# Kernel optimization log

Hardware: AMD Instinct MI355X
Metric: run time of the kernel (lower is better)

## Reference

```python
import jax, jax.numpy as jnp
import numpy as np

B, T, D, H, L, FF, SPLIT = 2, 4096, 256, 4 * 0 + 8, 4, 1024, 2048
HD = D // H
EPS = 1e-5


def _layernorm(x, s, b):
    mu = jnp.mean(x, axis=-1, keepdims=True)
    var = jnp.mean(jnp.square(x - mu), axis=-1, keepdims=True)
    return (x - mu) * jax.lax.rsqrt(var + EPS) * s + b


def setup_inputs() -> dict:
    key = jax.random.key(0)
    ks = jax.random.split(key, 10)
    sc = 0.02
    inp = {
        "rows": jax.random.normal(ks[0], (B, T, D), jnp.float32),
        "train_target_embeddings": jax.random.normal(ks[1], (B, SPLIT, D), jnp.float32),
        "Wq": sc * jax.random.normal(ks[2], (L, D, D), jnp.float32),
        "bq": jnp.zeros((L, D), jnp.float32),
        "Wk": sc * jax.random.normal(ks[3], (L, D, D), jnp.float32),
        "bk": jnp.zeros((L, D), jnp.float32),
        "Wv": sc * jax.random.normal(ks[4], (L, D, D), jnp.float32),
        "bv": jnp.zeros((L, D), jnp.float32),
        "Wo": sc * jax.random.normal(ks[5], (L, D, D), jnp.float32),
        "bo": jnp.zeros((L, D), jnp.float32),
        "W1": sc * jax.random.normal(ks[6], (L, D, FF), jnp.float32),
        "b1": jnp.zeros((L, FF), jnp.float32),
        "W2": sc * jax.random.normal(ks[7], (L, FF, D), jnp.float32),
        "b2": jnp.zeros((L, D), jnp.float32),
        "ln1_s": jnp.ones((L, D), jnp.float32),
        "ln1_b": jnp.zeros((L, D), jnp.float32),
        "ln2_s": jnp.ones((L, D), jnp.float32),
        "ln2_b": jnp.zeros((L, D), jnp.float32),
        "split": SPLIT,
    }
    return inp


def reference(rows, train_target_embeddings, Wq, bq, Wk, bk, Wv, bv, Wo, bo,
              W1, b1, W2, b2, ln1_s, ln1_b, ln2_s, ln2_b, split):
    # residual add of train target embeddings onto the train rows
    x = rows.at[:, :split, :].add(train_target_embeddings)
    t = x.shape[1]
    # allowed mask: every query can see all train columns; test queries also see themselves
    key_is_train = jnp.arange(t) < split                      # [T]
    allowed = key_is_train[None, :] | jnp.eye(t, dtype=bool)  # [T,T]
    neg = jnp.asarray(-1e9, x.dtype)
    scale = 1.0 / np.sqrt(HD)
    n_layers = Wq.shape[0]
    for l in range(n_layers):
        # multi-head attention with structured mask
        q = (x @ Wq[l] + bq[l]).reshape(x.shape[0], t, H, HD)
        k = (x @ Wk[l] + bk[l]).reshape(x.shape[0], t, H, HD)
        v = (x @ Wv[l] + bv[l]).reshape(x.shape[0], t, H, HD)
        logits = jnp.einsum('bqhd,bkhd->bhqk', q, k) * scale
        logits = jnp.where(allowed[None, None], logits, neg)
        attn = jax.nn.softmax(logits, axis=-1)
        o = jnp.einsum('bhqk,bkhd->bqhd', attn, v).reshape(x.shape[0], t, D)
        x = _layernorm(x + (o @ Wo[l] + bo[l]), ln1_s[l], ln1_b[l])
        # feed-forward
        h = jax.nn.gelu(x @ W1[l] + b1[l])
        x = _layernorm(x + (h @ W2[l] + b2[l]), ln2_s[l], ln2_b[l])
    return x
```

## Files before the change

### kernel.cpp

```cpp
#include <hip/hip_runtime.h>
#include <cstdint>
#include <cstddef>

#define TSEQ 4096
#define BATCH 2
#define DIM 256
#define NHEAD 8
#define HDIM 32
#define NLAYER 4
#define FFDIM 1024
#define SPLITN 2048
#define MROWS (BATCH * TSEQ)

#define QSCALE 0.2550784545f

typedef __attribute__((ext_vector_type(4))) float f32x4;
typedef __attribute__((ext_vector_type(8))) short bf16x8;

__device__ __forceinline__ short f2bf(float f) {
  union { float f; uint32_t u; } v; v.f = f;
  uint32_t r = v.u + 0x7fffu + ((v.u >> 16) & 1u);
  return (short)(r >> 16);
}

__device__ __forceinline__ float bf2f(short s) {
  union { uint32_t u; float f; } v; v.u = ((uint32_t)(uint16_t)s) << 16;
  return v.f;
}

__device__ __forceinline__ float fast_exp2(float x) {
#if __has_builtin(__builtin_amdgcn_exp2f)
  return __builtin_amdgcn_exp2f(x);
#else
  float r;
  asm volatile("v_exp_f32 %0, %1\n\ts_nop 1" : "=v"(r) : "v"(x));
  return r;
#endif
}

__device__ __forceinline__ uint32_t pack2bf(float a, float b) {
  union { float f; uint32_t u; } ua, ub; ua.f = a; ub.f = b;
  return ((ua.u + 0x8000u) >> 16) | ((ub.u + 0x8000u) & 0xffff0000u);
}

__device__ __forceinline__ bf16x8 mk8(uint32_t a, uint32_t b, uint32_t c, uint32_t d) {
  union { uint32_t u[4]; bf16x8 v; } x; x.u[0] = a; x.u[1] = b; x.u[2] = c; x.u[3] = d;
  return x.v;
}

__device__ __forceinline__ float gelu_f(float x) {
  float u = 0.7978845608f * x * (1.0f + 0.044715f * x * x);
  u = fminf(fmaxf(u, -20.f), 20.f);
  float e = fast_exp2(2.885390082f * u);
  float t = (e - 1.0f) / (e + 1.0f);
  return 0.5f * x * (1.0f + t);
}

#define AS1 __attribute__((address_space(1)))
#define AS3 __attribute__((address_space(3)))
__device__ __forceinline__ void gload16(const void* g, void* l) {
  __builtin_amdgcn_global_load_lds((AS1 void*)g, (AS3 void*)l, 16, 0, 0);
}

__global__ __launch_bounds__(256) void prep_w(
    const float* __restrict__ Wq, const float* __restrict__ Wk,
    const float* __restrict__ Wv, const float* __restrict__ Wo,
    const float* __restrict__ W1, const float* __restrict__ W2,
    short* __restrict__ qkvT, short* __restrict__ woT,
    short* __restrict__ w1T, short* __restrict__ w2T)
{
  const int NQKV = NLAYER * 768 * DIM;
  const int NO   = NLAYER * DIM * DIM;
  const int NF   = NLAYER * FFDIM * DIM;
  const int total = NQKV + NO + 2 * NF;
  for (int idx = blockIdx.x * 256 + threadIdx.x; idx < total; idx += gridDim.x * 256) {
    if (idx < NQKV) {
      const int l = idx / (768 * DIM);
      const int rem = idx - l * 768 * DIM;
      const int n = rem >> 8, k = rem & 255;
      const float* src = (n < 256) ? Wq : ((n < 512) ? Wk : Wv);
      qkvT[idx] = f2bf(src[((size_t)l * DIM + k) * DIM + (n & 255)]);
    } else if (idx < NQKV + NO) {
      const int j = idx - NQKV;
      const int l = j >> 16;
      const int rem = j & 65535;
      const int n = rem >> 8, k = rem & 255;
      woT[j] = f2bf(Wo[((size_t)l * DIM + k) * DIM + n]);
    } else if (idx < NQKV + NO + NF) {
      const int j = idx - NQKV - NO;
      const int l = j >> 18;
      const int rem = j & 262143;
      const int n = rem >> 8, k = rem & 255;
      w1T[j] = f2bf(W1[((size_t)l * DIM + k) * FFDIM + n]);
    } else {
      const int j = idx - NQKV - NO - NF;
      const int l = j >> 18;
      const int rem = j & 262143;
      const int n = rem >> 10, k = rem & 1023;
      w2T[j] = f2bf(W2[((size_t)l * FFDIM + k) * DIM + n]);
    }
  }
}

__global__ __launch_bounds__(256) void prep_x(
    const float* __restrict__ rows, const float* __restrict__ tte,
    float* __restrict__ xf, short* __restrict__ xb)
{
  const size_t idx = (size_t)blockIdx.x * 256 + threadIdx.x;
  float4 v = ((const float4*)rows)[idx];
  const size_t e = idx * 4;
  const int m = (int)(e >> 8);
  const int d = (int)(e & 255);
  const int t = m & (TSEQ - 1);
  const int bb = m >> 12;
  if (t < SPLITN) {
    const float4 a = ((const float4*)tte)[((size_t)bb * SPLITN + t) * (DIM / 4) + (d >> 2)];
    v.x += a.x; v.y += a.y; v.z += a.z; v.w += a.w;
  }
  ((float4*)xf)[idx] = v;
  short4 pk; pk.x = f2bf(v.x); pk.y = f2bf(v.y); pk.z = f2bf(v.z); pk.w = f2bf(v.w);
  ((short4*)xb)[idx] = pk;
}

#define GBM 128
#define GBN 64
#define GBK 64

template<int EPI>
__global__ __launch_bounds__(256, 4) void gemm_bt(
    const short* __restrict__ A, const short* __restrict__ BT,
    const float* __restrict__ bias0, const float* __restrict__ bias1,
    const float* __restrict__ bias2, void* __restrict__ Cout,
    int M, int N, int K)
{
  __shared__ short As[GBM * GBK];
  __shared__ short Bs[GBN * GBK];
  const int tid = threadIdx.x;
  const int lane = tid & 63;
  const int wave = tid >> 6;
  const int wm = wave & 1, wn = wave >> 1;
  const int col = lane & 15, quad = lane >> 4;

  const short* Ab = A + (size_t)blockIdx.x * GBM * K;
  const short* Bb = BT + (size_t)blockIdx.y * GBN * K;

  const f32x4 fz = {0.f, 0.f, 0.f, 0.f};
  f32x4 acc[4][2];
#pragma unroll
  for (int i = 0; i < 4; ++i)
#pragma unroll
    for (int j = 0; j < 2; ++j) acc[i][j] = fz;

  for (int k0 = 0; k0 < K; k0 += GBK) {
#pragma unroll
    for (int p = 0; p < 4; ++p) {
      const int i = p * 256 + tid;
      const int r = i >> 3, g = i & 7;
      gload16(Ab + (size_t)r * K + k0 + ((g ^ (r & 7)) * 8), &As[i * 8]);
    }
#pragma unroll
    for (int p = 0; p < 2; ++p) {
      const int i = p * 256 + tid;
      const int r = i >> 3, g = i & 7;
      gload16(Bb + (size_t)r * K + k0 + ((g ^ (r & 7)) * 8), &Bs[i * 8]);
    }
    __syncthreads();
#pragma unroll
    for (int ks = 0; ks < GBK; ks += 32) {
      bf16x8 af[4], bfr[2];
      const int gq = (ks >> 3) + quad;
#pragma unroll
      for (int tm = 0; tm < 4; ++tm) {
        const int row = wm * 64 + tm * 16 + col;
        af[tm] = *(const bf16x8*)&As[row * GBK + ((gq ^ (row & 7)) * 8)];
      }
#pragma unroll
      for (int tn = 0; tn < 2; ++tn) {
        const int row = wn * 32 + tn * 16 + col;
        bfr[tn] = *(const bf16x8*)&Bs[row * GBK + ((gq ^ (row & 7)) * 8)];
      }
#pragma unroll
      for (int tm = 0; tm < 4; ++tm)
#pragma unroll
        for (int tn = 0; tn < 2; ++tn)
          acc[tm][tn] = __builtin_amdgcn_mfma_f32_16x16x32_bf16(af[tm], bfr[tn], acc[tm][tn], 0, 0, 0);
    }
    __syncthreads();
  }

#pragma unroll
  for (int tm = 0; tm < 4; ++tm) {
    const int mbase = blockIdx.x * GBM + wm * 64 + tm * 16 + quad * 4;
#pragma unroll
    for (int tn = 0; tn < 2; ++tn) {
      const int n = blockIdx.y * GBN + wn * 32 + tn * 16 + col;
      float bv;
      if (EPI == 1) bv = (n < 256) ? bias0[n] : ((n < 512) ? bias1[n - 256] : bias2[n - 512]);
      else          bv = bias0[n];
#pragma unroll
      for (int r = 0; r < 4; ++r) {
        float v = acc[tm][tn][r] + bv;
        size_t off = (size_t)(mbase + r) * N + n;
        if (EPI == 1) {
          if (n < 256) v *= QSCALE;
          ((short*)Cout)[off] = f2bf(v);
        } else {
          ((short*)Cout)[off] = f2bf(gelu_f(v));
        }
      }
    }
  }
}

__global__ __launch_bounds__(256, 2) void gemm_ln(
    const short* __restrict__ A,
    const short* __restrict__ BT, const float* __restrict__ bias,
    const float* __restrict__ xres,
    const float* __restrict__ gs, const float* __restrict__ gb,
    float* __restrict__ xoutf, short* __restrict__ xoutb, int K)
{
  __shared__ short As[2][16 * 64];
  __shared__ short Bs[2][256 * 64];
  __shared__ float ssum[4][16], ssq[4][16];
  const int tid = threadIdx.x;
  const int lane = tid & 63;
  const int wave = tid >> 6;
  const int col = lane & 15, quad = lane >> 4;
  const int m0 = blockIdx.x * 16;

  const f32x4 fz = {0.f, 0.f, 0.f, 0.f};
  f32x4 acc[4];
#pragma unroll
  for (int j = 0; j < 4; ++j) acc[j] = fz;

  const int arow = (tid >> 3) & 15;
  const int agr  = tid & 7;
  const int grow = m0 + arow;
  const int asw  = (agr ^ (arow & 7)) * 8;

#define STAGE_B(k0_, buf_) do {                                              \
    _Pragma("unroll")                                                        \
    for (int p_ = 0; p_ < 8; ++p_) {                                         \
      const int i_ = p_ * 256 + tid;                                         \
      const int r_ = i_ >> 3, g_ = i_ & 7;                                   \
      gload16(BT + (size_t)r_ * K + (k0_) + ((g_ ^ (r_ & 7)) * 8),           \
              &Bs[buf_][i_ * 8]);                                            \
    } } while (0)

#define STAGE_A(k0_, buf_) do {                                              \
    if (tid < 128)                                                           \
      gload16(A + (size_t)grow * K + (k0_) + asw, &As[buf_][tid * 8]);       \
    } while (0)

  const int NT = K / 64;
  STAGE_B(0, 0);
  STAGE_A(0, 0);
  __syncthreads();

  int cur = 0;
  for (int t = 0; t < NT; ++t) {
    if (t + 1 < NT) {
      STAGE_B((t + 1) * 64, cur ^ 1);
      STAGE_A((t + 1) * 64, cur ^ 1);
    }
#pragma unroll
    for (int ks = 0; ks < 64; ks += 32) {
      bf16x8 af, bfr[4];
      const int gq = (ks >> 3) + quad;
      af = *(const bf16x8*)&As[cur][col * 64 + ((gq ^ (col & 7)) * 8)];
#pragma unroll
      for (int tn = 0; tn < 4; ++tn) {
        const int row = wave * 64 + tn * 16 + col;
        bfr[tn] = *(const bf16x8*)&Bs[cur][row * 64 + ((gq ^ (row & 7)) * 8)];
      }
#pragma unroll
      for (int tn = 0; tn < 4; ++tn)
        acc[tn] = __builtin_amdgcn_mfma_f32_16x16x32_bf16(af, bfr[tn], acc[tn], 0, 0, 0);
    }
    __syncthreads();
    cur ^= 1;
  }
#undef STAGE_B
#undef STAGE_A

  const float* resb = xres + (size_t)m0 * DIM;
#pragma unroll
  for (int tn = 0; tn < 4; ++tn) {
    const int n = wave * 64 + tn * 16 + col;
    const float bv = bias[n];
#pragma unroll
    for (int r = 0; r < 4; ++r) {
      const int row = quad * 4 + r;
      acc[tn][r] += bv + resb[(size_t)row * DIM + n];
    }
  }

#pragma unroll
  for (int r = 0; r < 4; ++r) {
    float s = 0.f, q = 0.f;
#pragma unroll
    for (int tn = 0; tn < 4; ++tn) { const float v = acc[tn][r]; s += v; q += v * v; }
    s += __shfl_xor(s, 1); q += __shfl_xor(q, 1);
    s += __shfl_xor(s, 2); q += __shfl_xor(q, 2);
    s += __shfl_xor(s, 4); q += __shfl_xor(q, 4);
    s += __shfl_xor(s, 8); q += __shfl_xor(q, 8);
    if (col == 0) { const int row = quad * 4 + r; ssum[wave][row] = s; ssq[wave][row] = q; }
  }
  __syncthreads();
  if (tid < 16) {
    const float S = ssum[0][tid] + ssum[1][tid] + ssum[2][tid] + ssum[3][tid];
    const float Q = ssq[0][tid] + ssq[1][tid] + ssq[2][tid] + ssq[3][tid];
    const float mu = S * (1.0f / DIM);
    const float var = Q * (1.0f / DIM) - mu * mu;
    ssum[0][tid] = mu;
    ssq[0][tid] = rsqrtf(var + 1e-5f);
  }
  __syncthreads();

#pragma unroll
  for (int tn = 0; tn < 4; ++tn) {
    const int n = wave * 64 + tn * 16 + col;
    const float g = gs[n], bb = gb[n];
#pragma unroll
    for (int r = 0; r < 4; ++r) {
      const int row = quad * 4 + r;
      const float out = (acc[tn][r] - ssum[0][row]) * ssq[0][row] * g + bb;
      xoutf[(size_t)(m0 + row) * DIM + n] = out;
      xoutb[(size_t)(m0 + row) * DIM + n] = f2bf(out);
    }
  }
}

#define AKT 64
#define NKT (SPLITN / AKT)

__global__ __launch_bounds__(256, 4) void attn_kernel(
    const short* __restrict__ qkv, short* __restrict__ ob)
{
  __shared__ short Kbuf[2][AKT * HDIM];
  __shared__ short Vbuf[2][HDIM * AKT];
  __shared__ float Pdiag[4][16];

  const int tid = threadIdx.x;
  const int lane = tid & 63;
  const int wave = tid >> 6;
  const int col = lane & 15, quad = lane >> 4;
  const int bh = blockIdx.y;
  const int b = bh >> 3, h = bh & 7;
  const int q0 = blockIdx.x * 128 + wave * 32;

  const short* qbase = qkv + (size_t)b * TSEQ * 768 + h * HDIM;
  const short* kbase = qbase + 256;
  const short* vcol  = qbase + 512;

  const short* ksrc = kbase + (size_t)(tid & 63) * 768 + (tid >> 6) * 8;
  const int vkey = tid & 63, vhg = tid >> 6;
  const int vs = vkey >> 4, vqd = (vkey >> 2) & 3, vrr = vkey & 3;
  const int vpos = (vs >> 1) * 32 + vqd * 8 + (vs & 1) * 4 + vrr;
  const int vgs = vpos >> 3, vo8 = vpos & 7;
  const short* vsrc = vcol + (size_t)vkey * 768 + vhg * 8;

  const bf16x8 qf0 = *(const bf16x8*)(qbase + (size_t)(q0 + col) * 768 + quad * 8);
  const bf16x8 qf1 = *(const bf16x8*)(qbase + (size_t)(q0 + 16 + col) * 768 + quad * 8);

  bf16x8 ones;
#pragma unroll
  for (int i = 0; i < 8; ++i) ones[i] = (short)0x3F80;

  const f32x4 fz = {0.f, 0.f, 0.f, 0.f};
  f32x4 o[2][2] = {{fz, fz}, {fz, fz}};
  f32x4 lacc[2] = {fz, fz};

  gload16(ksrc, &Kbuf[0][tid * 8]);
  {
    const bf16x8 v0 = *(const bf16x8*)vsrc;
#pragma unroll
    for (int j = 0; j < 8; ++j)
      Vbuf[0][(vhg * 8 + j) * 64 + ((vgs ^ j) * 8) + vo8] = v0[j];
  }
  bf16x8 vnext = *(const bf16x8*)(vsrc + (size_t)AKT * 768);

  int cur = 0;
  for (int t = 0; t < NKT; ++t) {
    __syncthreads();
    if (t + 1 < NKT) {
      gload16(ksrc + (size_t)(t + 1) * AKT * 768, &Kbuf[1 - cur][tid * 8]);
#pragma unroll
      for (int j = 0; j < 8; ++j)
        Vbuf[1 - cur][(vhg * 8 + j) * 64 + ((vgs ^ j) * 8) + vo8] = vnext[j];
      if (t + 2 < NKT) vnext = *(const bf16x8*)(vsrc + (size_t)(t + 2) * AKT * 768);
    }
    const short* kb = Kbuf[cur];
    const short* vb = Vbuf[cur];

    uint32_t pw0[8], pw1[8];
#pragma unroll
    for (int st = 0; st < 4; ++st) {
      const bf16x8 kf = *(const bf16x8*)&kb[(quad * 64 + st * 16 + col) * 8];
      const f32x4 s0 = __builtin_amdgcn_mfma_f32_16x16x32_bf16(kf, qf0, fz, 0, 0, 0);
      const f32x4 s1 = __builtin_amdgcn_mfma_f32_16x16x32_bf16(kf, qf1, fz, 0, 0, 0);
      pw0[st * 2]     = pack2bf(fast_exp2(s0[0]), fast_exp2(s0[1]));
      pw0[st * 2 + 1] = pack2bf(fast_exp2(s0[2]), fast_exp2(s0[3]));
      pw1[st * 2]     = pack2bf(fast_exp2(s1[0]), fast_exp2(s1[1]));
      pw1[st * 2 + 1] = pack2bf(fast_exp2(s1[2]), fast_exp2(s1[3]));
    }

#pragma unroll
    for (int kh = 0; kh < 2; ++kh) {
      const bf16x8 pf0 = mk8(pw0[kh * 4], pw0[kh * 4 + 1], pw0[kh * 4 + 2], pw0[kh * 4 + 3]);
      const bf16x8 pf1 = mk8(pw1[kh * 4], pw1[kh * 4 + 1], pw1[kh * 4 + 2], pw1[kh * 4 + 3]);
#pragma unroll
      for (int hh = 0; hh < 2; ++hh) {
        const int hd = hh * 16 + col;
        const bf16x8 vf = *(const bf16x8*)&vb[hd * AKT + (((kh * 4 + quad) ^ (hd & 7)) * 8)];
        o[0][hh] = __builtin_amdgcn_mfma_f32_16x16x32_bf16(pf0, vf, o[0][hh], 0, 0, 0);
        o[1][hh] = __builtin_amdgcn_mfma_f32_16x16x32_bf16(pf1, vf, o[1][hh], 0, 0, 0);
      }
      lacc[0] = __builtin_amdgcn_mfma_f32_16x16x32_bf16(pf0, ones, lacc[0], 0, 0, 0);
      lacc[1] = __builtin_amdgcn_mfma_f32_16x16x32_bf16(pf1, ones, lacc[1], 0, 0, 0);
    }
    cur ^= 1;
  }

  if (blockIdx.x >= SPLITN / 128) {
#pragma unroll
    for (int qsub = 0; qsub < 2; ++qsub) {
      const int qd = q0 + qsub * 16;
      const bf16x8 qf = qsub ? qf1 : qf0;
      const bf16x8 kf = *(const bf16x8*)(kbase + (size_t)(qd + col) * 768 + quad * 8);
      const f32x4 sd = __builtin_amdgcn_mfma_f32_16x16x32_bf16(kf, qf, fz, 0, 0, 0);
      float ps = 0.f;
#pragma unroll
      for (int r = 0; r < 4; ++r)
        if (quad * 4 + r == col) ps = fast_exp2(sd[r]);
      if (quad == (col >> 2)) Pdiag[wave][col] = ps;
      asm volatile("s_waitcnt lgkmcnt(0)" ::: "memory");
      const f32x4 pv = *(const f32x4*)&Pdiag[wave][quad * 4];
#pragma unroll
      for (int r = 0; r < 4; ++r) {
        lacc[qsub][r] += pv[r];
        const size_t vrow = (size_t)(qd + quad * 4 + r) * 768;
#pragma unroll
        for (int hh = 0; hh < 2; ++hh)
          o[qsub][hh][r] += pv[r] * bf2f(vcol[vrow + hh * 16 + col]);
      }
      asm volatile("s_waitcnt lgkmcnt(0)" ::: "memory");
    }
  }

#pragma unroll
  for (int qsub = 0; qsub < 2; ++qsub) {
#pragma unroll
    for (int r = 0; r < 4; ++r) {
      const float inv = 1.0f / lacc[qsub][r];
      const size_t row = (size_t)b * TSEQ + q0 + qsub * 16 + quad * 4 + r;
#pragma unroll
      for (int hh = 0; hh < 2; ++hh)
        ob[row * DIM + h * HDIM + hh * 16 + col] = f2bf(o[qsub][hh][r] * inv);
    }
  }
}

extern "C" void kernel_launch(void* const* d_in, const int* in_sizes, int n_in,
                              void* d_out, int out_size, void* d_ws, size_t ws_size,
                              hipStream_t stream)
{
  const float* rows = (const float*)d_in[0];
  const float* tte  = (const float*)d_in[1];
  const float* Wq = (const float*)d_in[2];  const float* bq = (const float*)d_in[3];
  const float* Wk = (const float*)d_in[4];  const float* bk = (const float*)d_in[5];
  const float* Wv = (const float*)d_in[6];  const float* bv = (const float*)d_in[7];
  const float* Wo = (const float*)d_in[8];  const float* bo = (const float*)d_in[9];
  const float* W1 = (const float*)d_in[10]; const float* b1 = (const float*)d_in[11];
  const float* W2 = (const float*)d_in[12]; const float* b2 = (const float*)d_in[13];
  const float* ln1s = (const float*)d_in[14]; const float* ln1b = (const float*)d_in[15];
  const float* ln2s = (const float*)d_in[16]; const float* ln2b = (const float*)d_in[17];

  char* p = (char*)d_ws;
  float* xf   = (float*)p;  p += (size_t)MROWS * DIM * 4;
  short* xb   = (short*)p;  p += (size_t)MROWS * DIM * 2;
  short* qkv  = (short*)p;  p += (size_t)MROWS * 768 * 2;
  short* hb   = (short*)p;  p += (size_t)MROWS * FFDIM * 2;
  short* ob   = (short*)p;  p += (size_t)MROWS * DIM * 2;
  short* qkvT = (short*)p;  p += (size_t)NLAYER * 768 * DIM * 2;
  short* woT  = (short*)p;  p += (size_t)NLAYER * DIM * DIM * 2;
  short* w1T  = (short*)p;  p += (size_t)NLAYER * FFDIM * DIM * 2;
  short* w2T  = (short*)p;  p += (size_t)NLAYER * DIM * FFDIM * 2;

  prep_w<<<2048, 256, 0, stream>>>(Wq, Wk, Wv, Wo, W1, W2, qkvT, woT, w1T, w2T);
  prep_x<<<MROWS * DIM / 4 / 256, 256, 0, stream>>>(rows, tte, xf, xb);

  for (int l = 0; l < NLAYER; ++l) {
    gemm_bt<1><<<dim3(MROWS / GBM, 768 / GBN), 256, 0, stream>>>(
        xb, qkvT + (size_t)l * 768 * DIM, bq + l * DIM, bk + l * DIM, bv + l * DIM,
        qkv, MROWS, 768, DIM);
    attn_kernel<<<dim3(TSEQ / 128, BATCH * NHEAD), 256, 0, stream>>>(qkv, ob);
    gemm_ln<<<MROWS / 16, 256, 0, stream>>>(
        ob, woT + (size_t)l * DIM * DIM, bo + l * DIM, xf,
        ln1s + l * DIM, ln1b + l * DIM, xf, xb, DIM);
    gemm_bt<3><<<dim3(MROWS / GBM, FFDIM / GBN), 256, 0, stream>>>(
        xb, w1T + (size_t)l * FFDIM * DIM, b1 + l * FFDIM, nullptr, nullptr,
        hb, MROWS, FFDIM, DIM);
    float* xo = (l == NLAYER - 1) ? (float*)d_out : xf;
    gemm_ln<<<MROWS / 16, 256, 0, stream>>>(
        hb, w2T + (size_t)l * DIM * FFDIM,
        b2 + l * DIM, xf, ln2s + l * DIM, ln2b + l * DIM, xo, xb, FFDIM);
  }
}
```

Before: 459.6 us.

## Software-pipeline attention: overlap next tile's QK^T with current PV

Restructures the attention main loop so the QK^T/exp stage for key tile t+1 runs in the same iteration as the PV accumulation for tile t. K is prefetched two tiles ahead and V is triple-buffered in shared memory, with the loop unrolled by two and ping-pong P register arrays. The goal is to hide LDS and global load latency and interleave exp work with MFMA work. The cost is more registers (the occupancy hint drops from 4 to 2 blocks) and extra shared memory.

```diff
diff --git a/kernel.cpp b/kernel.cpp
--- a/kernel.cpp
+++ b/kernel.cpp
@@ -334,11 +334,11 @@
 #define AKT 64
 #define NKT (SPLITN / AKT)
 
-__global__ __launch_bounds__(256, 4) void attn_kernel(
+__global__ __launch_bounds__(256, 2) void attn_kernel(
     const short* __restrict__ qkv, short* __restrict__ ob)
 {
   __shared__ short Kbuf[2][AKT * HDIM];
-  __shared__ short Vbuf[2][HDIM * AKT];
+  __shared__ short Vbuf[3][HDIM * AKT];
   __shared__ float Pdiag[4][16];
 
   const int tid = threadIdx.x;
@@ -371,56 +371,77 @@
   f32x4 o[2][2] = {{fz, fz}, {fz, fz}};
   f32x4 lacc[2] = {fz, fz};
 
+#define S_PHASE(KB, PN0, PN1) do {                                           \
+    _Pragma("unroll")                                                        \
+    for (int st = 0; st < 4; ++st) {                                         \
+      const bf16x8 kf = *(const bf16x8*)&(KB)[(quad * 64 + st * 16 + col) * 8]; \
+      const f32x4 s0 = __builtin_amdgcn_mfma_f32_16x16x32_bf16(kf, qf0, fz, 0, 0, 0); \
+      const f32x4 s1 = __builtin_amdgcn_mfma_f32_16x16x32_bf16(kf, qf1, fz, 0, 0, 0); \
+      (PN0)[st * 2]     = pack2bf(fast_exp2(s0[0]), fast_exp2(s0[1]));       \
+      (PN0)[st * 2 + 1] = pack2bf(fast_exp2(s0[2]), fast_exp2(s0[3]));       \
+      (PN1)[st * 2]     = pack2bf(fast_exp2(s1[0]), fast_exp2(s1[1]));       \
+      (PN1)[st * 2 + 1] = pack2bf(fast_exp2(s1[2]), fast_exp2(s1[3]));       \
+    } } while (0)
+
+#define PV_PHASE(VB, PC0, PC1) do {                                          \
+    _Pragma("unroll")                                                        \
+    for (int kh = 0; kh < 2; ++kh) {                                         \
+      const bf16x8 pf0 = mk8((PC0)[kh*4], (PC0)[kh*4+1], (PC0)[kh*4+2], (PC0)[kh*4+3]); \
+      const bf16x8 pf1 = mk8((PC1)[kh*4], (PC1)[kh*4+1], (PC1)[kh*4+2], (PC1)[kh*4+3]); \
+      _Pragma("unroll")                                                      \
+      for (int hh = 0; hh < 2; ++hh) {                                       \
+        const int hd = hh * 16 + col;                                        \
+        const bf16x8 vf = *(const bf16x8*)&(VB)[hd * AKT + (((kh * 4 + quad) ^ (hd & 7)) * 8)]; \
+        o[0][hh] = __builtin_amdgcn_mfma_f32_16x16x32_bf16(pf0, vf, o[0][hh], 0, 0, 0); \
+        o[1][hh] = __builtin_amdgcn_mfma_f32_16x16x32_bf16(pf1, vf, o[1][hh], 0, 0, 0); \
+      }                                                                      \
+      lacc[0] = __builtin_amdgcn_mfma_f32_16x16x32_bf16(pf0, ones, lacc[0], 0, 0, 0); \
+      lacc[1] = __builtin_amdgcn_mfma_f32_16x16x32_bf16(pf1, ones, lacc[1], 0, 0, 0); \
+    } } while (0)
+
+#define AITER(t_, PC0, PC1, PN0, PN1) do {                                   \
+    const int vnx = (vc >= 1) ? vc - 1 : 2;                    \
+    if ((t_) + 2 < NKT)                                                      \
+      gload16(ksrc + (size_t)((t_) + 2) * AKT * 768, &Kbuf[(t_) & 1][tid * 8]); \
+    if ((t_) + 1 < NKT) S_PHASE(Kbuf[((t_) + 1) & 1], PN0, PN1);             \
+    PV_PHASE(Vbuf[vc], PC0, PC1);                                            \
+    if ((t_) + 2 < NKT) {                                                    \
+      _Pragma("unroll")                                                      \
+      for (int j = 0; j < 8; ++j)                                            \
+        Vbuf[vnx][(vhg * 8 + j) * 64 + ((vgs ^ j) * 8) + vo8] = vreg[j];     \
+      if ((t_) + 3 < NKT)                                                    \
+        vreg = *(const bf16x8*)(vsrc + (size_t)((t_) + 3) * AKT * 768);      \
+    }                                                                        \
+    __syncthreads();                                                         \
+    vc = (vc == 2) ? 0 : vc + 1;                                             \
+  } while (0)
+
   gload16(ksrc, &Kbuf[0][tid * 8]);
+  gload16(ksrc + (size_t)AKT * 768, &Kbuf[1][tid * 8]);
   {
     const bf16x8 v0 = *(const bf16x8*)vsrc;
-#pragma unroll
-    for (int j = 0; j < 8; ++j)
+    const bf16x8 v1 = *(const bf16x8*)(vsrc + (size_t)AKT * 768);
+#pragma unroll
+    for (int j = 0; j < 8; ++j) {
       Vbuf[0][(vhg * 8 + j) * 64 + ((vgs ^ j) * 8) + vo8] = v0[j];
-  }
-  bf16x8 vnext = *(const bf16x8*)(vsrc + (size_t)AKT * 768);
-
-  int cur = 0;
-  for (int t = 0; t < NKT; ++t) {
-    __syncthreads();
-    if (t + 1 < NKT) {
-      gload16(ksrc + (size_t)(t + 1) * AKT * 768, &Kbuf[1 - cur][tid * 8]);
-#pragma unroll
-      for (int j = 0; j < 8; ++j)
-        Vbuf[1 - cur][(vhg * 8 + j) * 64 + ((vgs ^ j) * 8) + vo8] = vnext[j];
-      if (t + 2 < NKT) vnext = *(const bf16x8*)(vsrc + (size_t)(t + 2) * AKT * 768);
-    }
-    const short* kb = Kbuf[cur];
-    const short* vb = Vbuf[cur];
-
-    uint32_t pw0[8], pw1[8];
-#pragma unroll
-    for (int st = 0; st < 4; ++st) {
-      const bf16x8 kf = *(const bf16x8*)&kb[(quad * 64 + st * 16 + col) * 8];
-      const f32x4 s0 = __builtin_amdgcn_mfma_f32_16x16x32_bf16(kf, qf0, fz, 0, 0, 0);
-      const f32x4 s1 = __builtin_amdgcn_mfma_f32_16x16x32_bf16(kf, qf1, fz, 0, 0, 0);
-      pw0[st * 2]     = pack2bf(fast_exp2(s0[0]), fast_exp2(s0[1]));
-      pw0[st * 2 + 1] = pack2bf(fast_exp2(s0[2]), fast_exp2(s0[3]));
-      pw1[st * 2]     = pack2bf(fast_exp2(s1[0]), fast_exp2(s1[1]));
-      pw1[st * 2 + 1] = pack2bf(fast_exp2(s1[2]), fast_exp2(s1[3]));
-    }
-
-#pragma unroll
-    for (int kh = 0; kh < 2; ++kh) {
-      const bf16x8 pf0 = mk8(pw0[kh * 4], pw0[kh * 4 + 1], pw0[kh * 4 + 2], pw0[kh * 4 + 3]);
-      const bf16x8 pf1 = mk8(pw1[kh * 4], pw1[kh * 4 + 1], pw1[kh * 4 + 2], pw1[kh * 4 + 3]);
-#pragma unroll
-      for (int hh = 0; hh < 2; ++hh) {
-        const int hd = hh * 16 + col;
-        const bf16x8 vf = *(const bf16x8*)&vb[hd * AKT + (((kh * 4 + quad) ^ (hd & 7)) * 8)];
-        o[0][hh] = __builtin_amdgcn_mfma_f32_16x16x32_bf16(pf0, vf, o[0][hh], 0, 0, 0);
-        o[1][hh] = __builtin_amdgcn_mfma_f32_16x16x32_bf16(pf1, vf, o[1][hh], 0, 0, 0);
-      }
-      lacc[0] = __builtin_amdgcn_mfma_f32_16x16x32_bf16(pf0, ones, lacc[0], 0, 0, 0);
-      lacc[1] = __builtin_amdgcn_mfma_f32_16x16x32_bf16(pf1, ones, lacc[1], 0, 0, 0);
-    }
-    cur ^= 1;
-  }
+      Vbuf[1][(vhg * 8 + j) * 64 + ((vgs ^ j) * 8) + vo8] = v1[j];
+    }
+  }
+  bf16x8 vreg = *(const bf16x8*)(vsrc + (size_t)2 * AKT * 768);
+  __syncthreads();
+
+  uint32_t pwA0[8], pwA1[8], pwB0[8], pwB1[8];
+  S_PHASE(Kbuf[0], pwA0, pwA1);
+  __syncthreads();
+
+  int vc = 0;
+  for (int t = 0; t < NKT; t += 2) {
+    AITER(t,     pwA0, pwA1, pwB0, pwB1);
+    AITER(t + 1, pwB0, pwB1, pwA0, pwA1);
+  }
+#undef AITER
+#undef PV_PHASE
+#undef S_PHASE
 
   if (blockIdx.x >= SPLITN / 128) {
 #pragma unroll
```

After: 481.6 us. 1.05x slower.
